# Optimization experiments

Measured on AMD Instinct MI355X. Metric: run time of the kernel, lower is better.

Reference implementation:

```python
import jax, jax.numpy as jnp
import numpy as np

N_NODES = 10000
N_EDGES = 640000
IN, HID, OUT = 128, 256, 128


def setup_inputs() -> dict:
    key = jax.random.key(0)
    ks = jax.random.split(key, 8)
    scale_in = 1.0 / np.sqrt(IN)
    scale_hid = 1.0 / np.sqrt(HID)
    return {
        "x": jax.random.normal(ks[0], (N_NODES, IN), dtype=jnp.float32),
        "w_self1": jax.random.normal(ks[1], (IN, HID), dtype=jnp.float32) * scale_in,
        "w_neigh1": jax.random.normal(ks[2], (IN, HID), dtype=jnp.float32) * scale_in,
        "b1": jnp.zeros((HID,), dtype=jnp.float32),
        "w_self2": jax.random.normal(ks[3], (HID, OUT), dtype=jnp.float32) * scale_hid,
        "w_neigh2": jax.random.normal(ks[4], (HID, OUT), dtype=jnp.float32) * scale_hid,
        "b2": jnp.zeros((OUT,), dtype=jnp.float32),
        "src": jax.random.randint(ks[5], (N_EDGES,), 0, N_NODES, dtype=jnp.int64 if jax.config.jax_enable_x64 else jnp.int32),
        "dst": jax.random.randint(ks[6], (N_EDGES,), 0, N_NODES, dtype=jnp.int64 if jax.config.jax_enable_x64 else jnp.int32),
    }


def _mean_agg(h, src, dst, n_nodes):
    # gather source features along edges, segment-sum into destinations, divide by in-degree
    summed = jax.ops.segment_sum(h[src], dst, num_segments=n_nodes)  # [N, d]
    deg = jax.ops.segment_sum(jnp.ones_like(dst, dtype=h.dtype), dst, num_segments=n_nodes)
    return summed / jnp.maximum(deg, 1.0)[:, None]


def _sage_layer(h, src, dst, w_self, w_neigh, b):
    neigh = _mean_agg(h, src, dst, h.shape[0])
    return h @ w_self + neigh @ w_neigh + b


def reference(x, w_self1, w_neigh1, b1, w_self2, w_neigh2, b2, src, dst):
    h = _sage_layer(x, src, dst, w_self1, w_neigh1, b1)
    h = jax.nn.relu(h)  # dropout = identity in eval mode
    h = _sage_layer(h, src, dst, w_self2, w_neigh2, b2)
    return h
```

## Files before the change

kernel.cpp:

```cpp
#include <hip/hip_runtime.h>

#define N_NODES 10000
#define N_EDGES 640000
#define DIM_IN  128
#define DIM_HID 256
#define DIM_OUT 128
#define NPAD    10240
#define NBUCK   80
#define NPB     128
#define NBLKA   160
#define EPB     4000

typedef __attribute__((ext_vector_type(8))) short bf16x8;
typedef __attribute__((ext_vector_type(4))) float f32x4;

__device__ __forceinline__ unsigned short f2bf(float f) {
    unsigned int u = __float_as_uint(f);
    return (unsigned short)((u + 0x7fffu + ((u >> 16) & 1u)) >> 16);
}
__device__ __forceinline__ float bf2f(unsigned short h) {
    return __uint_as_float(((unsigned int)h) << 16);
}
__device__ __forceinline__ float bflo(unsigned int u) { return __uint_as_float(u << 16); }
__device__ __forceinline__ float bfhi(unsigned int u) { return __uint_as_float(u & 0xffff0000u); }

__global__ __launch_bounds__(256)
void countA_kernel(const int* __restrict__ dst, int* __restrict__ cntAT) {
    __shared__ int c[NBUCK];
    const int tid = threadIdx.x, blk = blockIdx.x;
    if (tid < NBUCK) c[tid] = 0;
    __syncthreads();
    const int e0 = blk * EPB;
    for (int i = tid; i < EPB; i += 256) atomicAdd(&c[dst[e0 + i] >> 7], 1);
    __syncthreads();
    if (tid < NBUCK) cntAT[tid * NBLKA + blk] = c[tid];
}

__global__ __launch_bounds__(64)
void scanB_kernel(const int* __restrict__ cntAT, int* __restrict__ runoffT) {
    const int lane = threadIdx.x;
    const int base = lane * (NBUCK * NBLKA / 64);
    int s = 0;
    for (int i = 0; i < NBUCK * NBLKA / 64; ++i) s += cntAT[base + i];
    int incl = s;
#pragma unroll
    for (int d = 1; d < 64; d <<= 1) {
        int u = __shfl_up(incl, d);
        if (lane >= d) incl += u;
    }
    int run = incl - s;
    for (int i = 0; i < NBUCK * NBLKA / 64; ++i) {
        runoffT[base + i] = run;
        run += cntAT[base + i];
    }
}

__global__ __launch_bounds__(256)
void scatterA_kernel(const int* __restrict__ src, const int* __restrict__ dst,
                     const int* __restrict__ runoffT, int* __restrict__ edges) {
    __shared__ int cur[NBUCK];
    const int tid = threadIdx.x, blk = blockIdx.x;
    if (tid < NBUCK) cur[tid] = runoffT[tid * NBLKA + blk];
    __syncthreads();
    const int e0 = blk * EPB;
    for (int i = tid; i < EPB; i += 256) {
        int s = src[e0 + i], d = dst[e0 + i];
        int pos = atomicAdd(&cur[d >> 7], 1);
        edges[pos] = (s << 7) | (d & (NPB - 1));
    }
}

__global__ __launch_bounds__(256)
void binB_kernel(const int* __restrict__ edges, const int* __restrict__ runoffT,
                 int* __restrict__ off, float* __restrict__ invdeg,
                 int* __restrict__ sorted_src) {
    __shared__ int cnt[NPB];
    __shared__ int curs[NPB];
    const int tid = threadIdx.x, b = blockIdx.x;
    const int base = runoffT[b * NBLKA];
    const int end  = (b == NBUCK - 1) ? N_EDGES : runoffT[(b + 1) * NBLKA];
    if (tid < NPB) cnt[tid] = 0;
    __syncthreads();
    for (int e = base + tid; e < end; e += 256) atomicAdd(&cnt[edges[e] & (NPB - 1)], 1);
    __syncthreads();
    if (tid < 64) {
        int c0 = cnt[tid * 2], c1 = cnt[tid * 2 + 1];
        int s = c0 + c1;
        int incl = s;
#pragma unroll
        for (int d = 1; d < 64; d <<= 1) {
            int u = __shfl_up(incl, d);
            if (tid >= d) incl += u;
        }
        int run = incl - s;
        curs[tid * 2] = run;
        curs[tid * 2 + 1] = run + c0;
    }
    __syncthreads();
    if (tid < NPB) {
        int n = b * NPB + tid;
        off[n] = base + curs[tid];
        if (n < N_NODES) invdeg[n] = 1.0f / fmaxf((float)cnt[tid], 1.0f);
        if (n == NPAD - 1) off[NPAD] = N_EDGES;
    }
    __syncthreads();
    for (int e = base + tid; e < end; e += 256) {
        int v = edges[e];
        int n = v & (NPB - 1);
        int pos = base + atomicAdd(&curs[n], 1);
        sorted_src[pos] = v >> 7;
    }
}

__global__ __launch_bounds__(256)
void prep_kernel(const float* __restrict__ x, unsigned short* __restrict__ xb,
                 const float* __restrict__ w1s, const float* __restrict__ w1n,
                 const float* __restrict__ w2s, const float* __restrict__ w2n,
                 unsigned short* __restrict__ o1s, unsigned short* __restrict__ o1n,
                 unsigned short* __restrict__ o2s, unsigned short* __restrict__ o2n) {
    const int tid = threadIdx.x, blk = blockIdx.x;
    if (blk < 1250) {
        int i = blk * 256 + tid;
        float4 v = ((const float4*)x)[i];
        ushort4 o;
        o.x = f2bf(v.x); o.y = f2bf(v.y); o.z = f2bf(v.z); o.w = f2bf(v.w);
        ((ushort4*)xb)[i] = o;
    } else {
        int which = (blk - 1250) >> 7;
        const float* w = (which == 0) ? w1s : (which == 1) ? w1n : (which == 2) ? w2s : w2n;
        unsigned short* o = (which == 0) ? o1s : (which == 1) ? o1n : (which == 2) ? o2s : o2n;
        int K = (which < 2) ? DIM_IN : DIM_HID;
        int N = (which < 2) ? DIM_HID : DIM_OUT;
        int idx = ((blk - 1250) & 127) * 256 + tid;
        int n = idx / K, k = idx - n * K;
        o[n * K + k] = f2bf(w[k * N + n]);
    }
}

__global__ __launch_bounds__(64)
void agg_kernel(const unsigned short* __restrict__ feat, const int* __restrict__ sorted_src,
                const int* __restrict__ off, const float* __restrict__ invdeg,
                unsigned short* __restrict__ outa) {
    const int n = blockIdx.x;
    const int lane = threadIdx.x;
    const int s0 = off[n], s1 = off[n + 1];
    __shared__ int sidx[64];
    float a0 = 0.f, b0 = 0.f, a1 = 0.f, b1 = 0.f;
    float a2 = 0.f, b2 = 0.f, a3 = 0.f, b3 = 0.f;
    for (int base = s0; base < s1; base += 64) {
        sidx[lane] = sorted_src[min(base + lane, s1 - 1)];
        __syncthreads();
        int c = min(64, s1 - base);
        int i = 0;
        for (; i + 4 <= c; i += 4) {
            unsigned int u0 = *(const unsigned int*)&feat[(size_t)sidx[i + 0] * 128 + 2 * lane];
            unsigned int u1 = *(const unsigned int*)&feat[(size_t)sidx[i + 1] * 128 + 2 * lane];
            unsigned int u2 = *(const unsigned int*)&feat[(size_t)sidx[i + 2] * 128 + 2 * lane];
            unsigned int u3 = *(const unsigned int*)&feat[(size_t)sidx[i + 3] * 128 + 2 * lane];
            a0 += bflo(u0); b0 += bfhi(u0);
            a1 += bflo(u1); b1 += bfhi(u1);
            a2 += bflo(u2); b2 += bfhi(u2);
            a3 += bflo(u3); b3 += bfhi(u3);
        }
        for (; i < c; ++i) {
            unsigned int u = *(const unsigned int*)&feat[(size_t)sidx[i] * 128 + 2 * lane];
            a0 += bflo(u); b0 += bfhi(u);
        }
        __syncthreads();
    }
    float inv = invdeg[n];
    float slo = ((a0 + a1) + (a2 + a3)) * inv;
    float shi = ((b0 + b1) + (b2 + b3)) * inv;
    unsigned int packed = (unsigned int)f2bf(slo) | ((unsigned int)f2bf(shi) << 16);
    *(unsigned int*)&outa[(size_t)n * 128 + 2 * lane] = packed;
}

template<int PASSES, bool RELU, bool OUT_BF16>
__launch_bounds__(256)
__global__ void mfma_gemm(const unsigned short* __restrict__ A1, const unsigned short* __restrict__ B1T,
                          const unsigned short* __restrict__ A2, const unsigned short* __restrict__ B2T,
                          const float* __restrict__ bias,
                          void* __restrict__ Cout, int M, int N, int K) {
    const int tid = threadIdx.x;
    const int w = tid >> 6, lane = tid & 63;
    const int m0 = blockIdx.x * 64, n0 = blockIdx.y * 64;
    const int l15 = lane & 15;
    const int koff = (lane >> 4) * 8;
    const int rowc = min(m0 + w * 16 + l15, M - 1);

    f32x4 acc[4] = {};
#pragma unroll
    for (int pass = 0; pass < PASSES; ++pass) {
        const unsigned short* __restrict__ A  = (PASSES == 2 && pass) ? A2 : A1;
        const unsigned short* __restrict__ BT = (PASSES == 2 && pass) ? B2T : B1T;
        const unsigned short* arow = A + (size_t)rowc * K;
        for (int k0 = 0; k0 < K; k0 += 32) {
            bf16x8 af = *(const bf16x8*)(arow + k0 + koff);
#pragma unroll
            for (int f = 0; f < 4; ++f) {
                const unsigned short* brow = BT + (size_t)(n0 + f * 16 + l15) * K;
                bf16x8 bfr = *(const bf16x8*)(brow + k0 + koff);
                acc[f] = __builtin_amdgcn_mfma_f32_16x16x32_bf16(af, bfr, acc[f], 0, 0, 0);
            }
        }
    }

#pragma unroll
    for (int f = 0; f < 4; ++f) {
        int col = n0 + f * 16 + l15;
        float bv = bias ? bias[col] : 0.f;
#pragma unroll
        for (int r = 0; r < 4; ++r) {
            int grow = m0 + w * 16 + (lane >> 4) * 4 + r;
            if (grow < M) {
                float v = acc[f][r] + bv;
                if (RELU) v = fmaxf(v, 0.f);
                if (OUT_BF16) ((unsigned short*)Cout)[(size_t)grow * N + col] = f2bf(v);
                else          ((float*)Cout)[(size_t)grow * N + col] = v;
            }
        }
    }
}

__launch_bounds__(256)
__global__ void gemm23_kernel(const unsigned short* __restrict__ A,
                              const unsigned short* __restrict__ BnT,
                              const unsigned short* __restrict__ BsT,
                              unsigned short* __restrict__ t, float* __restrict__ outbase,
                              int M, int N, int K) {
    const int tid = threadIdx.x;
    const int w = tid >> 6, lane = tid & 63;
    const int m0 = blockIdx.x * 64, n0 = blockIdx.y * 64;
    const int l15 = lane & 15;
    const int koff = (lane >> 4) * 8;
    const int rowc = min(m0 + w * 16 + l15, M - 1);

    f32x4 accn[4] = {};
    f32x4 accs[4] = {};
    const unsigned short* arow = A + (size_t)rowc * K;
    for (int k0 = 0; k0 < K; k0 += 32) {
        bf16x8 af = *(const bf16x8*)(arow + k0 + koff);
#pragma unroll
        for (int f = 0; f < 4; ++f) {
            const unsigned short* bnrow = BnT + (size_t)(n0 + f * 16 + l15) * K;
            const unsigned short* bsrow = BsT + (size_t)(n0 + f * 16 + l15) * K;
            bf16x8 bn = *(const bf16x8*)(bnrow + k0 + koff);
            bf16x8 bs = *(const bf16x8*)(bsrow + k0 + koff);
            accn[f] = __builtin_amdgcn_mfma_f32_16x16x32_bf16(af, bn, accn[f], 0, 0, 0);
            accs[f] = __builtin_amdgcn_mfma_f32_16x16x32_bf16(af, bs, accs[f], 0, 0, 0);
        }
    }

#pragma unroll
    for (int f = 0; f < 4; ++f) {
        int col = n0 + f * 16 + l15;
#pragma unroll
        for (int r = 0; r < 4; ++r) {
            int grow = m0 + w * 16 + (lane >> 4) * 4 + r;
            if (grow < M) {
                t[(size_t)grow * N + col]       = f2bf(accn[f][r]);
                outbase[(size_t)grow * N + col] = accs[f][r];
            }
        }
    }
}

__global__ __launch_bounds__(64)
void aggadd_kernel(const unsigned short* __restrict__ t, const int* __restrict__ sorted_src,
                   const int* __restrict__ off, const float* __restrict__ invdeg,
                   const float* __restrict__ outbase, const float* __restrict__ bias,
                   float* __restrict__ out) {
    const int n = blockIdx.x;
    const int lane = threadIdx.x;
    const int s0 = off[n], s1 = off[n + 1];
    __shared__ int sidx[64];
    float a0 = 0.f, b0 = 0.f, a1 = 0.f, b1 = 0.f;
    float a2 = 0.f, b2v = 0.f, a3 = 0.f, b3 = 0.f;
    for (int base = s0; base < s1; base += 64) {
        sidx[lane] = sorted_src[min(base + lane, s1 - 1)];
        __syncthreads();
        int c = min(64, s1 - base);
        int i = 0;
        for (; i + 4 <= c; i += 4) {
            unsigned int u0 = *(const unsigned int*)&t[(size_t)sidx[i + 0] * 128 + 2 * lane];
            unsigned int u1 = *(const unsigned int*)&t[(size_t)sidx[i + 1] * 128 + 2 * lane];
            unsigned int u2 = *(const unsigned int*)&t[(size_t)sidx[i + 2] * 128 + 2 * lane];
            unsigned int u3 = *(const unsigned int*)&t[(size_t)sidx[i + 3] * 128 + 2 * lane];
            a0 += bflo(u0); b0 += bfhi(u0);
            a1 += bflo(u1); b1 += bfhi(u1);
            a2 += bflo(u2); b2v += bfhi(u2);
            a3 += bflo(u3); b3 += bfhi(u3);
        }
        for (; i < c; ++i) {
            unsigned int u = *(const unsigned int*)&t[(size_t)sidx[i] * 128 + 2 * lane];
            a0 += bflo(u); b0 += bfhi(u);
        }
        __syncthreads();
    }
    float inv = invdeg[n];
    float slo = ((a0 + a1) + (a2 + a3)) * inv;
    float shi = ((b0 + b1) + (b2v + b3)) * inv;
    float2 ob = *(const float2*)&outbase[(size_t)n * 128 + 2 * lane];
    float2 o;
    o.x = (ob.x + bias[2 * lane])     + slo;
    o.y = (ob.y + bias[2 * lane + 1]) + shi;
    *(float2*)&out[(size_t)n * 128 + 2 * lane] = o;
}

extern "C" void kernel_launch(void* const* d_in, const int* in_sizes, int n_in,
                              void* d_out, int out_size, void* d_ws, size_t ws_size,
                              hipStream_t stream) {
    const float* x        = (const float*)d_in[0];
    const float* w_self1  = (const float*)d_in[1];
    const float* w_neigh1 = (const float*)d_in[2];
    const float* b1       = (const float*)d_in[3];
    const float* w_self2  = (const float*)d_in[4];
    const float* w_neigh2 = (const float*)d_in[5];
    const float* b2       = (const float*)d_in[6];
    const int*   src      = (const int*)d_in[7];
    const int*   dst      = (const int*)d_in[8];
    float* out = (float*)d_out;

    char* p = (char*)d_ws;
    auto alloc = [&](size_t bytes) { char* q = p; p += (bytes + 1023) & ~(size_t)1023; return q; };
    int*            cntAT      = (int*)alloc(NBUCK * NBLKA * 4);
    int*            runoffT    = (int*)alloc(NBUCK * NBLKA * 4);
    int*            edges      = (int*)alloc((size_t)N_EDGES * 4);
    int*            off        = (int*)alloc((NPAD + 1) * 4);
    int*            sorted_src = (int*)alloc((size_t)N_EDGES * 4);
    float*          invdeg     = (float*)alloc(NPAD * 4);
    unsigned short* xb         = (unsigned short*)alloc((size_t)N_NODES * DIM_IN * 2);
    unsigned short* w1sT       = (unsigned short*)alloc(DIM_IN * DIM_HID * 2);
    unsigned short* w1nT       = (unsigned short*)alloc(DIM_IN * DIM_HID * 2);
    unsigned short* w2sT       = (unsigned short*)alloc(DIM_HID * DIM_OUT * 2);
    unsigned short* w2nT       = (unsigned short*)alloc(DIM_HID * DIM_OUT * 2);
    unsigned short* aggbuf     = (unsigned short*)alloc((size_t)N_NODES * 128 * 2);
    unsigned short* h          = (unsigned short*)alloc((size_t)N_NODES * DIM_HID * 2);
    unsigned short* t          = (unsigned short*)alloc((size_t)N_NODES * DIM_OUT * 2);
    float*          outbase    = (float*)alloc((size_t)N_NODES * DIM_OUT * 4);

    countA_kernel  <<<NBLKA, 256, 0, stream>>>(dst, cntAT);
    scanB_kernel   <<<1, 64, 0, stream>>>(cntAT, runoffT);
    scatterA_kernel<<<NBLKA, 256, 0, stream>>>(src, dst, runoffT, edges);
    binB_kernel    <<<NBUCK, 256, 0, stream>>>(edges, runoffT, off, invdeg, sorted_src);

    prep_kernel<<<1250 + 512, 256, 0, stream>>>(x, xb, w_self1, w_neigh1, w_self2, w_neigh2,
                                                w1sT, w1nT, w2sT, w2nT);

    agg_kernel<<<N_NODES, 64, 0, stream>>>(xb, sorted_src, off, invdeg, aggbuf);
    mfma_gemm<2, true, true><<<dim3(157, DIM_HID / 64), 256, 0, stream>>>(
        xb, w1sT, aggbuf, w1nT, b1, h, N_NODES, DIM_HID, DIM_IN);

    gemm23_kernel<<<dim3(157, DIM_OUT / 64), 256, 0, stream>>>(
        h, w2nT, w2sT, t, outbase, N_NODES, DIM_OUT, DIM_HID);
    aggadd_kernel<<<N_NODES, 64, 0, stream>>>(t, sorted_src, off, invdeg, outbase, b2, out);
}
```

Baseline: 185.1 us.

## Fuse prep with bucket count, split binning per wave, unroll gathers by eight

The bf16 conversion/transposition kernel and the bucket-count kernel become a single launch, which removes one kernel launch and lets both kinds of work share the GPU. The binning kernel now gives each of its four waves its own quarter of the edges, with per-wave histograms and cursors, to cut shared-memory atomic contention. The offset and inverse-degree writes are folded into the scan step. Both gather loops are unrolled from four to eight loads to keep more memory requests in flight, at the cost of more registers and a longer scalar tail loop.

```diff
diff --git a/kernel.cpp b/kernel.cpp
--- a/kernel.cpp
+++ b/kernel.cpp
@@ -25,15 +25,38 @@
 __device__ __forceinline__ float bfhi(unsigned int u) { return __uint_as_float(u & 0xffff0000u); }
 
 __global__ __launch_bounds__(256)
-void countA_kernel(const int* __restrict__ dst, int* __restrict__ cntAT) {
+void prepc_kernel(const float* __restrict__ x, unsigned short* __restrict__ xb,
+                  const float* __restrict__ w1s, const float* __restrict__ w1n,
+                  const float* __restrict__ w2s, const float* __restrict__ w2n,
+                  unsigned short* __restrict__ o1s, unsigned short* __restrict__ o1n,
+                  unsigned short* __restrict__ o2s, unsigned short* __restrict__ o2n,
+                  const int* __restrict__ dst, int* __restrict__ cntAT) {
     __shared__ int c[NBUCK];
     const int tid = threadIdx.x, blk = blockIdx.x;
-    if (tid < NBUCK) c[tid] = 0;
-    __syncthreads();
-    const int e0 = blk * EPB;
-    for (int i = tid; i < EPB; i += 256) atomicAdd(&c[dst[e0 + i] >> 7], 1);
-    __syncthreads();
-    if (tid < NBUCK) cntAT[tid * NBLKA + blk] = c[tid];
+    if (blk < 1250) {
+        int i = blk * 256 + tid;
+        float4 v = ((const float4*)x)[i];
+        ushort4 o;
+        o.x = f2bf(v.x); o.y = f2bf(v.y); o.z = f2bf(v.z); o.w = f2bf(v.w);
+        ((ushort4*)xb)[i] = o;
+    } else if (blk < 1762) {
+        int which = (blk - 1250) >> 7;
+        const float* w = (which == 0) ? w1s : (which == 1) ? w1n : (which == 2) ? w2s : w2n;
+        unsigned short* o = (which == 0) ? o1s : (which == 1) ? o1n : (which == 2) ? o2s : o2n;
+        int K = (which < 2) ? DIM_IN : DIM_HID;
+        int N = (which < 2) ? DIM_HID : DIM_OUT;
+        int idx = ((blk - 1250) & 127) * 256 + tid;
+        int n = idx / K, k = idx - n * K;
+        o[n * K + k] = f2bf(w[k * N + n]);
+    } else {
+        int ablk = blk - 1762;
+        if (tid < NBUCK) c[tid] = 0;
+        __syncthreads();
+        const int e0 = ablk * EPB;
+        for (int i = tid; i < EPB; i += 256) atomicAdd(&c[dst[e0 + i] >> 7], 1);
+        __syncthreads();
+        if (tid < NBUCK) cntAT[tid * NBLKA + ablk] = c[tid];
+    }
 }
 
 __global__ __launch_bounds__(64)
@@ -74,66 +97,55 @@
 void binB_kernel(const int* __restrict__ edges, const int* __restrict__ runoffT,
                  int* __restrict__ off, float* __restrict__ invdeg,
                  int* __restrict__ sorted_src) {
-    __shared__ int cnt[NPB];
-    __shared__ int curs[NPB];
+    __shared__ int cnt[4][NPB];
+    __shared__ int curs[4][NPB];
     const int tid = threadIdx.x, b = blockIdx.x;
+    const int w = tid >> 6, lane = tid & 63;
     const int base = runoffT[b * NBLKA];
     const int end  = (b == NBUCK - 1) ? N_EDGES : runoffT[(b + 1) * NBLKA];
-    if (tid < NPB) cnt[tid] = 0;
+    const int len  = end - base;
+    const int q0 = base + (len * w) / 4;
+    const int q1 = base + (len * (w + 1)) / 4;
+    cnt[w][lane] = 0; cnt[w][lane + 64] = 0;
     __syncthreads();
-    for (int e = base + tid; e < end; e += 256) atomicAdd(&cnt[edges[e] & (NPB - 1)], 1);
+    for (int e = q0 + lane; e < q1; e += 64) atomicAdd(&cnt[w][edges[e] & (NPB - 1)], 1);
     __syncthreads();
-    if (tid < 64) {
-        int c0 = cnt[tid * 2], c1 = cnt[tid * 2 + 1];
-        int s = c0 + c1;
+    if (w == 0) {
+        int n0 = 2 * lane, n1 = 2 * lane + 1;
+        int c00 = cnt[0][n0], c10 = cnt[1][n0], c20 = cnt[2][n0], c30 = cnt[3][n0];
+        int c01 = cnt[0][n1], c11 = cnt[1][n1], c21 = cnt[2][n1], c31 = cnt[3][n1];
+        int t0 = c00 + c10 + c20 + c30;
+        int t1 = c01 + c11 + c21 + c31;
+        int s = t0 + t1;
         int incl = s;
 #pragma unroll
         for (int d = 1; d < 64; d <<= 1) {
             int u = __shfl_up(incl, d);
-            if (tid >= d) incl += u;
+            if (lane >= d) incl += u;
         }
         int run = incl - s;
-        curs[tid * 2] = run;
-        curs[tid * 2 + 1] = run + c0;
+        int g0 = b * NPB + n0, g1 = b * NPB + n1;
+        off[g0] = base + run;
+        off[g1] = base + run + t0;
+        if (g0 < N_NODES) invdeg[g0] = 1.0f / fmaxf((float)t0, 1.0f);
+        if (g1 < N_NODES) invdeg[g1] = 1.0f / fmaxf((float)t1, 1.0f);
+        if (g1 == NPAD - 1) off[NPAD] = N_EDGES;
+        curs[0][n0] = base + run;
+        curs[1][n0] = base + run + c00;
+        curs[2][n0] = base + run + c00 + c10;
+        curs[3][n0] = base + run + c00 + c10 + c20;
+        int r1 = run + t0;
+        curs[0][n1] = base + r1;
+        curs[1][n1] = base + r1 + c01;
+        curs[2][n1] = base + r1 + c01 + c11;
+        curs[3][n1] = base + r1 + c01 + c11 + c21;
     }
     __syncthreads();
-    if (tid < NPB) {
-        int n = b * NPB + tid;
-        off[n] = base + curs[tid];
-        if (n < N_NODES) invdeg[n] = 1.0f / fmaxf((float)cnt[tid], 1.0f);
-        if (n == NPAD - 1) off[NPAD] = N_EDGES;
-    }
-    __syncthreads();
-    for (int e = base + tid; e < end; e += 256) {
+    for (int e = q0 + lane; e < q1; e += 64) {
         int v = edges[e];
         int n = v & (NPB - 1);
-        int pos = base + atomicAdd(&curs[n], 1);
+        int pos = atomicAdd(&curs[w][n], 1);
         sorted_src[pos] = v >> 7;
-    }
-}
-
-__global__ __launch_bounds__(256)
-void prep_kernel(const float* __restrict__ x, unsigned short* __restrict__ xb,
-                 const float* __restrict__ w1s, const float* __restrict__ w1n,
-                 const float* __restrict__ w2s, const float* __restrict__ w2n,
-                 unsigned short* __restrict__ o1s, unsigned short* __restrict__ o1n,
-                 unsigned short* __restrict__ o2s, unsigned short* __restrict__ o2n) {
-    const int tid = threadIdx.x, blk = blockIdx.x;
-    if (blk < 1250) {
-        int i = blk * 256 + tid;
-        float4 v = ((const float4*)x)[i];
-        ushort4 o;
-        o.x = f2bf(v.x); o.y = f2bf(v.y); o.z = f2bf(v.z); o.w = f2bf(v.w);
-        ((ushort4*)xb)[i] = o;
-    } else {
-        int which = (blk - 1250) >> 7;
-        const float* w = (which == 0) ? w1s : (which == 1) ? w1n : (which == 2) ? w2s : w2n;
-        unsigned short* o = (which == 0) ? o1s : (which == 1) ? o1n : (which == 2) ? o2s : o2n;
-        int K = (which < 2) ? DIM_IN : DIM_HID;
-        int N = (which < 2) ? DIM_HID : DIM_OUT;
-        int idx = ((blk - 1250) & 127) * 256 + tid;
-        int n = idx / K, k = idx - n * K;
-        o[n * K + k] = f2bf(w[k * N + n]);
     }
 }
 
@@ -152,15 +164,23 @@
         __syncthreads();
         int c = min(64, s1 - base);
         int i = 0;
-        for (; i + 4 <= c; i += 4) {
+        for (; i + 8 <= c; i += 8) {
             unsigned int u0 = *(const unsigned int*)&feat[(size_t)sidx[i + 0] * 128 + 2 * lane];
             unsigned int u1 = *(const unsigned int*)&feat[(size_t)sidx[i + 1] * 128 + 2 * lane];
             unsigned int u2 = *(const unsigned int*)&feat[(size_t)sidx[i + 2] * 128 + 2 * lane];
             unsigned int u3 = *(const unsigned int*)&feat[(size_t)sidx[i + 3] * 128 + 2 * lane];
+            unsigned int u4 = *(const unsigned int*)&feat[(size_t)sidx[i + 4] * 128 + 2 * lane];
+            unsigned int u5 = *(const unsigned int*)&feat[(size_t)sidx[i + 5] * 128 + 2 * lane];
+            unsigned int u6 = *(const unsigned int*)&feat[(size_t)sidx[i + 6] * 128 + 2 * lane];
+            unsigned int u7 = *(const unsigned int*)&feat[(size_t)sidx[i + 7] * 128 + 2 * lane];
             a0 += bflo(u0); b0 += bfhi(u0);
             a1 += bflo(u1); b1 += bfhi(u1);
             a2 += bflo(u2); b2 += bfhi(u2);
             a3 += bflo(u3); b3 += bfhi(u3);
+            a0 += bflo(u4); b0 += bfhi(u4);
+            a1 += bflo(u5); b1 += bfhi(u5);
+            a2 += bflo(u6); b2 += bfhi(u6);
+            a3 += bflo(u7); b3 += bfhi(u7);
         }
         for (; i < c; ++i) {
             unsigned int u = *(const unsigned int*)&feat[(size_t)sidx[i] * 128 + 2 * lane];
@@ -281,15 +301,23 @@
         __syncthreads();
         int c = min(64, s1 - base);
         int i = 0;
-        for (; i + 4 <= c; i += 4) {
+        for (; i + 8 <= c; i += 8) {
             unsigned int u0 = *(const unsigned int*)&t[(size_t)sidx[i + 0] * 128 + 2 * lane];
             unsigned int u1 = *(const unsigned int*)&t[(size_t)sidx[i + 1] * 128 + 2 * lane];
             unsigned int u2 = *(const unsigned int*)&t[(size_t)sidx[i + 2] * 128 + 2 * lane];
             unsigned int u3 = *(const unsigned int*)&t[(size_t)sidx[i + 3] * 128 + 2 * lane];
+            unsigned int u4 = *(const unsigned int*)&t[(size_t)sidx[i + 4] * 128 + 2 * lane];
+            unsigned int u5 = *(const unsigned int*)&t[(size_t)sidx[i + 5] * 128 + 2 * lane];
+            unsigned int u6 = *(const unsigned int*)&t[(size_t)sidx[i + 6] * 128 + 2 * lane];
+            unsigned int u7 = *(const unsigned int*)&t[(size_t)sidx[i + 7] * 128 + 2 * lane];
             a0 += bflo(u0); b0 += bfhi(u0);
             a1 += bflo(u1); b1 += bfhi(u1);
             a2 += bflo(u2); b2v += bfhi(u2);
             a3 += bflo(u3); b3 += bfhi(u3);
+            a0 += bflo(u4); b0 += bfhi(u4);
+            a1 += bflo(u5); b1 += bfhi(u5);
+            a2 += bflo(u6); b2v += bfhi(u6);
+            a3 += bflo(u7); b3 += bfhi(u7);
         }
         for (; i < c; ++i) {
             unsigned int u = *(const unsigned int*)&t[(size_t)sidx[i] * 128 + 2 * lane];
@@ -339,14 +367,13 @@
     unsigned short* t          = (unsigned short*)alloc((size_t)N_NODES * DIM_OUT * 2);
     float*          outbase    = (float*)alloc((size_t)N_NODES * DIM_OUT * 4);
 
-    countA_kernel  <<<NBLKA, 256, 0, stream>>>(dst, cntAT);
+    prepc_kernel<<<1250 + 512 + NBLKA, 256, 0, stream>>>(
+        x, xb, w_self1, w_neigh1, w_self2, w_neigh2, w1sT, w1nT, w2sT, w2nT, dst, cntAT);
+
     scanB_kernel   <<<1, 64, 0, stream>>>(cntAT, runoffT);
     scatterA_kernel<<<NBLKA, 256, 0, stream>>>(src, dst, runoffT, edges);
     binB_kernel    <<<NBUCK, 256, 0, stream>>>(edges, runoffT, off, invdeg, sorted_src);
 
-    prep_kernel<<<1250 + 512, 256, 0, stream>>>(x, xb, w_self1, w_neigh1, w_self2, w_neigh2,
-                                                w1sT, w1nT, w2sT, w2nT);
-
     agg_kernel<<<N_NODES, 64, 0, stream>>>(xb, sorted_src, off, invdeg, aggbuf);
     mfma_gemm<2, true, true><<<dim3(157, DIM_HID / 64), 256, 0, stream>>>(
         xb, w1sT, aggbuf, w1nT, b1, h, N_NODES, DIM_HID, DIM_IN);
```

New measurement: 182.0 us. Within noise of the previous version (-1.7%).
